# Kernel optimization log

Hardware: AMD Instinct MI355X
Metric: run time of the kernel (lower is better)

Reference implementation:

```python
import jax, jax.numpy as jnp
import numpy as np

N_NODES = 25000
N_EDGES = 50000
NUM_ATOMS = 26
HID = 64
EMB = 64
N_GRAPHS = 64
NUM_NN_ITER = 3


def setup_inputs() -> dict:
    key = jax.random.key(0)
    ks = jax.random.split(key, 16)

    def nrm(k, shape, s=0.1):
        return jax.random.normal(k, shape, dtype=jnp.float32) * s

    x = jax.random.uniform(ks[0], (N_NODES, NUM_ATOMS), dtype=jnp.float32)
    edge_index = jax.random.randint(ks[1], (2, N_EDGES), 0, N_NODES)
    edge_attr = jax.random.uniform(ks[2], (N_EDGES, 4), dtype=jnp.float32)
    batch = jnp.sort(jax.random.randint(ks[3], (N_NODES,), 0, N_GRAPHS))

    params = dict(
        W_in=nrm(ks[4], (NUM_ATOMS, HID)), b_in=jnp.zeros((HID,), jnp.float32),
        We1=nrm(ks[5], (4, 128)), be1=jnp.zeros((128,), jnp.float32),
        We2=nrm(ks[6], (128, HID * HID), 0.02), be2=jnp.zeros((HID * HID,), jnp.float32),
        W_root=nrm(ks[7], (HID, HID)), b_conv=jnp.zeros((HID,), jnp.float32),
        W_ih=nrm(ks[8], (3 * HID, HID)), b_ih=jnp.zeros((3 * HID,), jnp.float32),
        W_hh=nrm(ks[9], (3 * HID, HID)), b_hh=jnp.zeros((3 * HID,), jnp.float32),
        Wo1=nrm(ks[10], (HID, HID)), bo1=jnp.zeros((HID,), jnp.float32),
        Wo2=nrm(ks[11], (HID, EMB)), bo2=jnp.zeros((EMB,), jnp.float32),
        Wp=nrm(ks[12], (EMB + NUM_ATOMS, 1)), bp=jnp.zeros((1,), jnp.float32),
    )
    return {"x": x, "edge_index": edge_index, "edge_attr": edge_attr, "batch": batch, **params}


def reference(x, edge_index, edge_attr, batch,
              W_in, b_in, We1, be1, We2, be2, W_root, b_conv,
              W_ih, b_ih, W_hh, b_hh, Wo1, bo1, Wo2, bo2, Wp, bp):
    src, dst = edge_index[0], edge_index[1]
    # edge MLP -> per-edge (HID, HID) weight blocks; edge_attr is fixed so compute once
    Wedge = (jax.nn.relu(edge_attr @ We1 + be1) @ We2 + be2).reshape(-1, HID, HID)  # (E, h, h)

    out = jax.nn.relu(x @ W_in + b_in)  # (N, h)
    h = out
    for _ in range(NUM_NN_ITER):
        # NNConv (aggr='add'): root transform + gather->bmm->scatter_add
        msg = jnp.einsum('ei,eio->eo', out[src], Wedge)           # (E, h)
        agg = jax.ops.segment_sum(msg, dst, num_segments=N_NODES)  # (N, h)
        m = jax.nn.relu(out @ W_root + agg + b_conv)
        # single-step GRU cell (torch GRU equations)
        gi = m @ W_ih.T + b_ih
        gh = h @ W_hh.T + b_hh
        i_r, i_z, i_n = jnp.split(gi, 3, axis=-1)
        h_r, h_z, h_n = jnp.split(gh, 3, axis=-1)
        r = jax.nn.sigmoid(i_r + h_r)
        z = jax.nn.sigmoid(i_z + h_z)
        n = jnp.tanh(i_n + r * h_n)
        h = (1.0 - z) * n + z * h
        out = h

    o = jax.nn.relu(out @ Wo1 + bo1) @ Wo2 + bo2            # (N, EMB)
    feat = jnp.concatenate([o, x], axis=1)                  # (N, EMB + NUM_ATOMS)
    # F.normalize: row-wise L2 with eps clamp
    feat = feat / jnp.maximum(jnp.linalg.norm(feat, axis=1, keepdims=True), 1e-12)
    # scatter_mean readout over graphs
    cnt = jax.ops.segment_sum(jnp.ones((N_NODES,), jnp.float32), batch, num_segments=N_GRAPHS)
    readout = jax.ops.segment_sum(feat, batch, num_segments=N_GRAPHS) / jnp.maximum(cnt, 1.0)[:, None]
    ratio = jax.nn.sigmoid(readout @ Wp + bp)               # (G, 1)
    return feat, ratio
```

## Files before the change

kernel.cpp:

```cpp
#include <hip/hip_runtime.h>
#include <math.h>

#define NN 25000
#define NE 50000
#define NEP2 50176
#define NATOM 26
#define NUM_ITER 3
#define NCH 33
#define NPB 32
#define EB2 512
#define KSP 17

typedef __attribute__((ext_vector_type(8))) short bf16x8;
typedef __attribute__((ext_vector_type(8))) unsigned short ushort8_t;
typedef __attribute__((ext_vector_type(4))) float f32x4;
union FragU { bf16x8 v; ushort4 q[2]; };

static __device__ __forceinline__ ushort f2bf(float f) {
  unsigned u = __float_as_uint(f);
  unsigned r = (u + 0x7FFFu + ((u >> 16) & 1u)) >> 16;
  return (ushort)r;
}
static __device__ __forceinline__ unsigned cvt_pk_bf16(float a, float b) {
  unsigned r;
  asm("v_cvt_pk_bf16_f32 %0, %1, %2" : "=v"(r) : "v"(a), "v"(b));
  return r;
}
static __device__ __forceinline__ float bflo(unsigned u) { return __uint_as_float(u << 16); }
static __device__ __forceinline__ float bfhi(unsigned u) { return __uint_as_float(u & 0xFFFF0000u); }

__global__ __launch_bounds__(256) void edge_mlp_pack_kernel(
    const float* __restrict__ ea, const float* __restrict__ We1,
    const float* __restrict__ be1, ushort* __restrict__ Upkt) {
  int t = threadIdx.x;
  int el = t & 63, seg = t >> 6;
  int e = blockIdx.x * 64 + el;
  bool valid = (e < NE);
  float a0 = 0.f, a1 = 0.f, a2 = 0.f, a3 = 0.f;
  if (valid) { a0 = ea[e * 4]; a1 = ea[e * 4 + 1]; a2 = ea[e * 4 + 2]; a3 = ea[e * 4 + 3]; }
  #pragma unroll
  for (int q = 0; q < 8; ++q) {
    int g = seg * 8 + q;
    ushort out[4];
    #pragma unroll
    for (int kk = 0; kk < 4; ++kk) {
      int k = g * 4 + kk;
      float v = be1[k];
      v = fmaf(a0, We1[k], v);
      v = fmaf(a1, We1[128 + k], v);
      v = fmaf(a2, We1[256 + k], v);
      v = fmaf(a3, We1[384 + k], v);
      out[kk] = valid ? f2bf(fmaxf(v, 0.f)) : (ushort)0;
    }
    *(ushort4*)&Upkt[((size_t)g * NEP2 + e) * 4] = *(ushort4*)out;
  }
  if (seg == 0) {
    ushort out[4] = {(ushort)(valid ? 0x3F80 : 0), 0, 0, 0};
    *(ushort4*)&Upkt[((size_t)32 * NEP2 + e) * 4] = *(ushort4*)out;
  }
}

__global__ __launch_bounds__(256) void bpk_pack_kernel(
    const float* __restrict__ We2, const float* __restrict__ be2,
    ushort* __restrict__ Bpk) {
  int idx = blockIdx.x * 256 + threadIdx.x;
  int lane = idx & 63;
  int nt = (idx >> 6) & 3;
  int ks = (idx >> 8) & 7;
  int c = idx >> 11;
  int l15 = lane & 15, lg = lane >> 4;
  int o = nt * 16 + l15;
  ushort v[8];
  #pragma unroll
  for (int j = 0; j < 8; ++j) {
    int kl = (j < 4) ? (4 * lg + j) : (12 + 4 * lg + j);
    int f = c * 256 + ks * 32 + kl;
    int k = f >> 6, i = f & 63;
    float wv = 0.f;
    if (k < 128) wv = We2[(size_t)k * 4096 + i * 64 + o];
    else if (k == 128) wv = be2[i * 64 + o];
    v[j] = f2bf(wv);
  }
  *(ushort8_t*)(Bpk + (size_t)idx * 8) = *(ushort8_t*)v;
}

__global__ __launch_bounds__(256) void nw_pack_kernel(
    const float* __restrict__ W_root, const float* __restrict__ W_ih,
    const float* __restrict__ W_hh, ushort* __restrict__ Wr_pk,
    ushort* __restrict__ Bih_pk, ushort* __restrict__ Bhh_pk) {
  int idx = blockIdx.x * 256 + threadIdx.x;
  if (idx >= 3584) return;
  int lane, nt, ks, kind;
  ushort* dstp;
  if (idx < 512)      { kind = 0; int f = idx;        lane = f & 63; nt = (f >> 6) % 4;  ks = (f >> 6) / 4;  dstp = Wr_pk  + (size_t)f * 8; }
  else if (idx < 2048){ kind = 1; int f = idx - 512;  lane = f & 63; nt = (f >> 6) % 12; ks = (f >> 6) / 12; dstp = Bih_pk + (size_t)f * 8; }
  else                { kind = 2; int f = idx - 2048; lane = f & 63; nt = (f >> 6) % 12; ks = (f >> 6) / 12; dstp = Bhh_pk + (size_t)f * 8; }
  int l15 = lane & 15, lg = lane >> 4;
  int col = nt * 16 + l15;
  ushort v[8];
  #pragma unroll
  for (int j = 0; j < 8; ++j) {
    int kl = (j < 4) ? (4 * lg + j) : (12 + 4 * lg + j);
    int i = ks * 32 + kl;
    float wv;
    if (kind == 0)      wv = W_root[i * 64 + col];
    else if (kind == 1) wv = W_ih[col * 64 + i];
    else                wv = W_hh[col * 64 + i];
    v[j] = f2bf(wv);
  }
  *(ushort8_t*)dstp = *(ushort8_t*)v;
}

__global__ __launch_bounds__(512, 2) void edge_rgemm2_kernel(
    const ushort* __restrict__ Upkt, const ushort* __restrict__ Bpk,
    const float* __restrict__ hv, const int* __restrict__ src,
    const int* __restrict__ dst, float* __restrict__ agg) {
  __shared__ ushort sB[2][16384];
  __shared__ ushort sU[2][2048];
  __shared__ ushort sS[512][72];
  int tid = threadIdx.x;
  int lane = tid & 63, w = tid >> 6;
  int l15 = lane & 15, lg = lane >> 4;
  int e0 = blockIdx.x * EB2;
  int c0 = blockIdx.y * KSP;
  int c1 = (c0 + KSP < NCH) ? (c0 + KSP) : NCH;

  #pragma unroll
  for (int r = 0; r < 16; ++r) {
    int idx = r * 512 + tid;
    int el = idx >> 4, part = idx & 15;
    int e = e0 + el;
    float4 v = make_float4(0.f, 0.f, 0.f, 0.f);
    if (e < NE) v = ((const float4*)hv)[(size_t)src[e] * 16 + part];
    unsigned lo = cvt_pk_bf16(v.x, v.y);
    unsigned hi = cvt_pk_bf16(v.z, v.w);
    *(uint2*)&sS[el][part * 4] = make_uint2(lo, hi);
  }

  ushort8_t rB[4]; uint2 rU;
  {
    const ushort* bs = Bpk + (size_t)c0 * 16384;
    #pragma unroll
    for (int r = 0; r < 4; ++r)
      rB[r] = *(const ushort8_t*)(bs + ((size_t)r * 512 + tid) * 8);
    rU = *(const uint2*)(Upkt + ((size_t)c0 * NEP2 + e0) * 4 + tid * 4);
  }
  #pragma unroll
  for (int r = 0; r < 4; ++r)
    *(ushort8_t*)&sB[0][((size_t)r * 512 + tid) * 8] = rB[r];
  *(uint2*)&sU[0][tid * 4] = rU;
  __syncthreads();

  float4 sreg[4][2][2];
  #pragma unroll
  for (int mt = 0; mt < 4; ++mt)
    #pragma unroll
    for (int p = 0; p < 2; ++p)
      #pragma unroll
      for (int g = 0; g < 2; ++g) {
        uint2 d = *(const uint2*)&sS[w * 64 + mt * 16 + l15][p * 32 + g * 16 + 4 * lg];
        sreg[mt][p][g] = make_float4(bflo(d.x), bfhi(d.x), bflo(d.y), bfhi(d.y));
      }

  f32x4 acc[4][4];
  #pragma unroll
  for (int mt = 0; mt < 4; ++mt)
    #pragma unroll
    for (int nt = 0; nt < 4; ++nt) acc[mt][nt] = (f32x4){0.f, 0.f, 0.f, 0.f};

  for (int c = c0; c < c1; ++c) {
    int cur = (c - c0) & 1;
    bool more = (c + 1 < c1);
    if (more) {
      const ushort* bs = Bpk + (size_t)(c + 1) * 16384;
      #pragma unroll
      for (int r = 0; r < 4; ++r)
        rB[r] = *(const ushort8_t*)(bs + ((size_t)r * 512 + tid) * 8);
      rU = *(const uint2*)(Upkt + ((size_t)(c + 1) * NEP2 + e0) * 4 + tid * 4);
    }
    float uu[4][4];
    #pragma unroll
    for (int mt = 0; mt < 4; ++mt) {
      uint2 d = *(const uint2*)&sU[cur][(w * 64 + mt * 16 + l15) * 4];
      uu[mt][0] = bflo(d.x); uu[mt][1] = bfhi(d.x);
      uu[mt][2] = bflo(d.y); uu[mt][3] = bfhi(d.y);
    }
    #pragma unroll
    for (int ks = 0; ks < 8; ++ks) {
      int p = ks & 1, ku = ks >> 1;
      bf16x8 bfr[4];
      #pragma unroll
      for (int nt = 0; nt < 4; ++nt)
        bfr[nt] = *(const bf16x8*)&sB[cur][(((size_t)ks * 4 + nt) * 64 + lane) * 8];
      #pragma unroll
      for (int mt = 0; mt < 4; ++mt) {
        float u = uu[mt][ku];
        float4 s0 = sreg[mt][p][0], s1 = sreg[mt][p][1];
        union { bf16x8 v; unsigned u32[4]; } af;
        af.u32[0] = cvt_pk_bf16(s0.x * u, s0.y * u);
        af.u32[1] = cvt_pk_bf16(s0.z * u, s0.w * u);
        af.u32[2] = cvt_pk_bf16(s1.x * u, s1.y * u);
        af.u32[3] = cvt_pk_bf16(s1.z * u, s1.w * u);
        #pragma unroll
        for (int nt = 0; nt < 4; ++nt)
          acc[mt][nt] = __builtin_amdgcn_mfma_f32_16x16x32_bf16(af.v, bfr[nt], acc[mt][nt], 0, 0, 0);
      }
    }
    if (more) {
      int nb = cur ^ 1;
      #pragma unroll
      for (int r = 0; r < 4; ++r)
        *(ushort8_t*)&sB[nb][((size_t)r * 512 + tid) * 8] = rB[r];
      *(uint2*)&sU[nb][tid * 4] = rU;
    }
    __syncthreads();
  }

  #pragma unroll
  for (int mt = 0; mt < 4; ++mt) {
    #pragma unroll
    for (int rr = 0; rr < 4; ++rr) {
      int e = e0 + w * 64 + mt * 16 + lg * 4 + rr;
      if (e < NE) {
        int d = dst[e];
        #pragma unroll
        for (int nt = 0; nt < 4; ++nt)
          atomicAdd(&agg[(size_t)d * 64 + nt * 16 + l15], acc[mt][nt][rr]);
      }
    }
  }
}

__global__ __launch_bounds__(256) void node_in_kernel(
    const float* __restrict__ x, const float* __restrict__ W_in,
    const float* __restrict__ b_in, float* __restrict__ h) {
  int idx = blockIdx.x * 256 + threadIdx.x;
  if (idx >= NN * 64) return;
  int n = idx >> 6, c = idx & 63;
  float acc = b_in[c];
  #pragma unroll
  for (int j = 0; j < NATOM; ++j) acc = fmaf(x[n * NATOM + j], W_in[j * 64 + c], acc);
  h[idx] = fmaxf(acc, 0.f);
}

__global__ __launch_bounds__(256, 1) void node_update2_kernel(
    float* __restrict__ hv, const float* __restrict__ agg,
    const ushort* __restrict__ Wr_pk, const ushort* __restrict__ Bih_pk,
    const ushort* __restrict__ Bhh_pk, const float* __restrict__ b_conv,
    const float* __restrict__ b_ih, const float* __restrict__ b_hh) {
  __shared__ ushort h_lds[128][72];
  __shared__ ushort m_lds[128][72];
  int tid = threadIdx.x;
  int lane = tid & 63, w = tid >> 6;
  int l15 = lane & 15, lg = lane >> 4;
  int n0 = blockIdx.x * 128;

  #pragma unroll
  for (int r = 0; r < 8; ++r) {
    int idx = r * 256 + tid;
    int row = idx >> 4, part = idx & 15;
    int n = n0 + row;
    float4 v = make_float4(0.f, 0.f, 0.f, 0.f);
    if (n < NN) v = ((const float4*)hv)[(size_t)n * 16 + part];
    *(uint2*)&h_lds[row][part * 4] =
        make_uint2(cvt_pk_bf16(v.x, v.y), cvt_pk_bf16(v.z, v.w));
  }
  __syncthreads();

  bf16x8 ah[2][2];
  #pragma unroll
  for (int mt = 0; mt < 2; ++mt)
    #pragma unroll
    for (int ks = 0; ks < 2; ++ks) {
      int row = w * 32 + mt * 16 + l15;
      FragU f;
      f.q[0] = *(const ushort4*)&h_lds[row][ks * 32 + 4 * lg];
      f.q[1] = *(const ushort4*)&h_lds[row][ks * 32 + 16 + 4 * lg];
      ah[mt][ks] = f.v;
    }

  f32x4 accm[2][4];
  #pragma unroll
  for (int mt = 0; mt < 2; ++mt)
    #pragma unroll
    for (int nt = 0; nt < 4; ++nt) accm[mt][nt] = (f32x4){0.f, 0.f, 0.f, 0.f};
  #pragma unroll
  for (int ks = 0; ks < 2; ++ks)
    #pragma unroll
    for (int nt = 0; nt < 4; ++nt) {
      bf16x8 b = *(const bf16x8*)(Wr_pk + ((size_t)((ks * 4 + nt) * 64 + lane)) * 8);
      #pragma unroll
      for (int mt = 0; mt < 2; ++mt)
        accm[mt][nt] = __builtin_amdgcn_mfma_f32_16x16x32_bf16(ah[mt][ks], b, accm[mt][nt], 0, 0, 0);
    }
  #pragma unroll
  for (int mt = 0; mt < 2; ++mt)
    #pragma unroll
    for (int nt = 0; nt < 4; ++nt) {
      int col = nt * 16 + l15;
      float bc = b_conv[col];
      #pragma unroll
      for (int rr = 0; rr < 4; ++rr) {
        int row = w * 32 + mt * 16 + lg * 4 + rr;
        int n = n0 + row;
        float val = 0.f;
        if (n < NN) val = fmaxf(accm[mt][nt][rr] + agg[(size_t)n * 64 + col] + bc, 0.f);
        m_lds[row][col] = f2bf(val);
      }
    }
  __syncthreads();

  bf16x8 am[2][2];
  #pragma unroll
  for (int mt = 0; mt < 2; ++mt)
    #pragma unroll
    for (int ks = 0; ks < 2; ++ks) {
      int row = w * 32 + mt * 16 + l15;
      FragU f;
      f.q[0] = *(const ushort4*)&m_lds[row][ks * 32 + 4 * lg];
      f.q[1] = *(const ushort4*)&m_lds[row][ks * 32 + 16 + 4 * lg];
      am[mt][ks] = f.v;
    }

  f32x4 acc_s[2][8], acc_in[2][4], acc_hn[2][4];
  #pragma unroll
  for (int mt = 0; mt < 2; ++mt) {
    #pragma unroll
    for (int nt = 0; nt < 8; ++nt) acc_s[mt][nt] = (f32x4){0.f, 0.f, 0.f, 0.f};
    #pragma unroll
    for (int nt = 0; nt < 4; ++nt) {
      acc_in[mt][nt] = (f32x4){0.f, 0.f, 0.f, 0.f};
      acc_hn[mt][nt] = (f32x4){0.f, 0.f, 0.f, 0.f};
    }
  }
  #pragma unroll
  for (int ks = 0; ks < 2; ++ks) {
    #pragma unroll
    for (int nt = 0; nt < 8; ++nt) {
      bf16x8 bi = *(const bf16x8*)(Bih_pk + ((size_t)((ks * 12 + nt) * 64 + lane)) * 8);
      bf16x8 bh = *(const bf16x8*)(Bhh_pk + ((size_t)((ks * 12 + nt) * 64 + lane)) * 8);
      #pragma unroll
      for (int mt = 0; mt < 2; ++mt) {
        acc_s[mt][nt] = __builtin_amdgcn_mfma_f32_16x16x32_bf16(am[mt][ks], bi, acc_s[mt][nt], 0, 0, 0);
        acc_s[mt][nt] = __builtin_amdgcn_mfma_f32_16x16x32_bf16(ah[mt][ks], bh, acc_s[mt][nt], 0, 0, 0);
      }
    }
    #pragma unroll
    for (int nt = 8; nt < 12; ++nt) {
      bf16x8 bi = *(const bf16x8*)(Bih_pk + ((size_t)((ks * 12 + nt) * 64 + lane)) * 8);
      bf16x8 bh = *(const bf16x8*)(Bhh_pk + ((size_t)((ks * 12 + nt) * 64 + lane)) * 8);
      #pragma unroll
      for (int mt = 0; mt < 2; ++mt) {
        acc_in[mt][nt - 8] = __builtin_amdgcn_mfma_f32_16x16x32_bf16(am[mt][ks], bi, acc_in[mt][nt - 8], 0, 0, 0);
        acc_hn[mt][nt - 8] = __builtin_amdgcn_mfma_f32_16x16x32_bf16(ah[mt][ks], bh, acc_hn[mt][nt - 8], 0, 0, 0);
      }
    }
  }

  #pragma unroll
  for (int mt = 0; mt < 2; ++mt)
    #pragma unroll
    for (int nt = 0; nt < 4; ++nt) {
      int col = nt * 16 + l15;
      float b_sr = b_ih[col] + b_hh[col];
      float b_sz = b_ih[64 + col] + b_hh[64 + col];
      float b_in_ = b_ih[128 + col];
      float b_hn = b_hh[128 + col];
      #pragma unroll
      for (int rr = 0; rr < 4; ++rr) {
        int row = w * 32 + mt * 16 + lg * 4 + rr;
        int n = n0 + row;
        if (n >= NN) continue;
        float Sr = acc_s[mt][nt][rr] + b_sr;
        float Sz = acc_s[mt][nt + 4][rr] + b_sz;
        float vin = acc_in[mt][nt][rr] + b_in_;
        float vhn = acc_hn[mt][nt][rr] + b_hn;
        float r = 1.f / (1.f + __expf(-Sr));
        float z = 1.f / (1.f + __expf(-Sz));
        float nn = tanhf(fmaf(r, vhn, vin));
        float hp = hv[(size_t)n * 64 + col];
        hv[(size_t)n * 64 + col] = (1.f - z) * nn + z * hp;
      }
    }
}

__global__ __launch_bounds__(256) void head2_kernel(
    const float* __restrict__ hv, const float* __restrict__ x,
    const float* __restrict__ Wo1, const float* __restrict__ bo1,
    const float* __restrict__ Wo2, const float* __restrict__ bo2,
    float* __restrict__ feat) {
  __shared__ float wo1[64 * 64];
  __shared__ float wo2[64 * 64];
  __shared__ float s_row[NPB * 64];
  __shared__ float s_o1[NPB * 64];
  int tid = threadIdx.x;
  int n0 = blockIdx.x * NPB;

  for (int idx = tid; idx < 64 * 16; idx += 256) {
    ((float4*)wo1)[idx] = ((const float4*)Wo1)[idx];
    ((float4*)wo2)[idx] = ((const float4*)Wo2)[idx];
  }
  for (int idx = tid; idx < NPB * 64; idx += 256) {
    int n = n0 + (idx >> 6);
    s_row[idx] = (n < NN) ? hv[(size_t)n * 64 + (idx & 63)] : 0.f;
  }
  __syncthreads();

  int c = tid & 63, g = tid >> 6;
  #pragma unroll
  for (int q = 0; q < 8; ++q) {
    int nl = g + 4 * q;
    float a = bo1[c];
    for (int i = 0; i < 64; ++i) a = fmaf(s_row[nl * 64 + i], wo1[i * 64 + c], a);
    s_o1[nl * 64 + c] = fmaxf(a, 0.f);
  }
  __syncthreads();
  #pragma unroll
  for (int q = 0; q < 8; ++q) {
    int nl = g + 4 * q;
    int n = n0 + nl;
    float b = bo2[c];
    for (int i = 0; i < 64; ++i) b = fmaf(s_o1[nl * 64 + i], wo2[i * 64 + c], b);
    float xv = (c < NATOM && n < NN) ? x[(size_t)n * NATOM + c] : 0.f;
    float sq = b * b + xv * xv;
    #pragma unroll
    for (int off = 1; off < 64; off <<= 1) sq += __shfl_xor(sq, off);
    if (n >= NN) continue;
    float inv = 1.f / fmaxf(sqrtf(sq), 1e-12f);
    feat[(size_t)n * 90 + c] = b * inv;
    if (c < NATOM) feat[(size_t)n * 90 + 64 + c] = xv * inv;
  }
}

static __device__ __forceinline__ int lbound(const int* __restrict__ b, int v) {
  int lo = 0, hi = NN;
  while (lo < hi) { int m = (lo + hi) >> 1; if (b[m] < v) lo = m + 1; else hi = m; }
  return lo;
}

__global__ __launch_bounds__(128) void readout_kernel(
    const float* __restrict__ feat, const int* __restrict__ batch,
    float* __restrict__ readout, float* __restrict__ cnt) {
  __shared__ int bounds[2];
  int g = blockIdx.x;
  int t = threadIdx.x;
  if (t == 0) bounds[0] = lbound(batch, g);
  if (t == 1) bounds[1] = lbound(batch, g + 1);
  __syncthreads();
  int lo = bounds[0], hi = bounds[1];
  if (t < 90) {
    float a0 = 0.f, a1 = 0.f, a2 = 0.f, a3 = 0.f;
    int n = lo;
    for (; n + 3 < hi; n += 4) {
      a0 += feat[(size_t)n * 90 + t];
      a1 += feat[(size_t)(n + 1) * 90 + t];
      a2 += feat[(size_t)(n + 2) * 90 + t];
      a3 += feat[(size_t)(n + 3) * 90 + t];
    }
    for (; n < hi; ++n) a0 += feat[(size_t)n * 90 + t];
    readout[g * 90 + t] = (a0 + a1) + (a2 + a3);
  }
  if (t == 0) cnt[g] = (float)(hi - lo);
}

__global__ __launch_bounds__(64) void ratio_kernel(
    const float* __restrict__ readout, const float* __restrict__ cnt,
    const float* __restrict__ Wp, const float* __restrict__ bp,
    float* __restrict__ ratio) {
  int g = threadIdx.x;
  float c = fmaxf(cnt[g], 1.f);
  float a = bp[0];
  for (int j = 0; j < 90; ++j) a = fmaf(readout[g * 90 + j] / c, Wp[j], a);
  ratio[g] = 1.f / (1.f + __expf(-a));
}


extern "C" void kernel_launch(void* const* d_in, const int* in_sizes, int n_in,
                              void* d_out, int out_size, void* d_ws, size_t ws_size,
                              hipStream_t stream) {
  const float* x      = (const float*)d_in[0];
  const int*   ei     = (const int*)  d_in[1];
  const float* ea     = (const float*)d_in[2];
  const int*   batch  = (const int*)  d_in[3];
  const float* W_in   = (const float*)d_in[4];
  const float* b_in   = (const float*)d_in[5];
  const float* We1    = (const float*)d_in[6];
  const float* be1    = (const float*)d_in[7];
  const float* We2    = (const float*)d_in[8];
  const float* be2    = (const float*)d_in[9];
  const float* W_root = (const float*)d_in[10];
  const float* b_conv = (const float*)d_in[11];
  const float* W_ih   = (const float*)d_in[12];
  const float* b_ih   = (const float*)d_in[13];
  const float* W_hh   = (const float*)d_in[14];
  const float* b_hh   = (const float*)d_in[15];
  const float* Wo1    = (const float*)d_in[16];
  const float* bo1    = (const float*)d_in[17];
  const float* Wo2    = (const float*)d_in[18];
  const float* bo2    = (const float*)d_in[19];
  const float* Wp     = (const float*)d_in[20];
  const float* bp     = (const float*)d_in[21];

  const int* srcp = ei;
  const int* dstp = ei + NE;
  float* feat  = (float*)d_out;
  float* ratio = feat + (size_t)NN * 90;

  char* wsb = (char*)d_ws;
  ushort* Upkt   = (ushort*)(wsb + 0);
  ushort* Bpk    = (ushort*)(wsb + 13246464);
  float*  h      = (float*) (wsb + 14327808);
  float*  agg    = (float*) (wsb + 20727808);
  float*  readout= (float*) (wsb + 27127808);
  float*  cnt    = (float*) (wsb + 27150848);
  ushort* Wr_pk  = (ushort*)(wsb + 27151104);
  ushort* Bih_pk = (ushort*)(wsb + 27159296);
  ushort* Bhh_pk = (ushort*)(wsb + 27183872);

  edge_mlp_pack_kernel<<<NEP2 / 64, 256, 0, stream>>>(ea, We1, be1, Upkt);
  bpk_pack_kernel<<<(NCH * 8 * 4 * 64) / 256, 256, 0, stream>>>(We2, be2, Bpk);
  nw_pack_kernel<<<14, 256, 0, stream>>>(W_root, W_ih, W_hh, Wr_pk, Bih_pk, Bhh_pk);
  node_in_kernel<<<(NN * 64 + 255) / 256, 256, 0, stream>>>(x, W_in, b_in, h);

  for (int it = 0; it < NUM_ITER; ++it) {
    hipMemsetAsync(agg, 0, (size_t)NN * 64 * sizeof(float), stream);
    edge_rgemm2_kernel<<<dim3(NEP2 / EB2, 2), 512, 0, stream>>>(
        Upkt, Bpk, h, srcp, dstp, agg);
    node_update2_kernel<<<(NN + 127) / 128, 256, 0, stream>>>(
        h, agg, Wr_pk, Bih_pk, Bhh_pk, b_conv, b_ih, b_hh);
  }

  head2_kernel<<<(NN + NPB - 1) / NPB, 256, 0, stream>>>(
      h, x, Wo1, bo1, Wo2, bo2, feat);
  readout_kernel<<<64, 128, 0, stream>>>(feat, batch, readout, cnt);
  ratio_kernel<<<1, 64, 0, stream>>>(readout, cnt, Wp, bp, ratio);
}
```

Measured before the change: 441.6 us.

## Restructure edge GEMM: factor U scaling out of MFMA, split output columns, async LDS loads

The edge-conditioned GEMM kernel is reorganised. Source features are converted to bf16 fragments once, kept in registers, and reused as MFMA A operands. The per-edge U coefficient is applied as an fp32 FMA on the MFMA result, which removes the per-k rescale and bf16 conversion of A. Output columns are split across a new grid z dimension so each block handles 32 columns, halving LDS and accumulator use and allowing 4 blocks per CU. B tiles are double-buffered with global_load_lds, and U is read straight from global memory. The cost is twice as many MFMAs per useful output (two chained MFMAs plus an FMA per tile), a doubled source-row gather across the column halves, and extra fp32 FMAs.

```diff
diff --git a/kernel.cpp b/kernel.cpp
--- a/kernel.cpp
+++ b/kernel.cpp
@@ -15,6 +15,10 @@
 typedef __attribute__((ext_vector_type(8))) unsigned short ushort8_t;
 typedef __attribute__((ext_vector_type(4))) float f32x4;
 union FragU { bf16x8 v; ushort4 q[2]; };
+
+#define GLDS16(gp, lp) __builtin_amdgcn_global_load_lds( \
+    (const __attribute__((address_space(1))) void*)(gp), \
+    (__attribute__((address_space(3))) void*)(lp), 16, 0, 0)
 
 static __device__ __forceinline__ ushort f2bf(float f) {
   unsigned u = __float_as_uint(f);
@@ -111,107 +115,94 @@
   *(ushort8_t*)dstp = *(ushort8_t*)v;
 }
 
-__global__ __launch_bounds__(512, 2) void edge_rgemm2_kernel(
+__global__ __launch_bounds__(512, 4) void edge_rgemm5_kernel(
     const ushort* __restrict__ Upkt, const ushort* __restrict__ Bpk,
     const float* __restrict__ hv, const int* __restrict__ src,
     const int* __restrict__ dst, float* __restrict__ agg) {
-  __shared__ ushort sB[2][16384];
-  __shared__ ushort sU[2][2048];
-  __shared__ ushort sS[512][72];
+  __shared__ ushort sB[2][8192];
   int tid = threadIdx.x;
   int lane = tid & 63, w = tid >> 6;
   int l15 = lane & 15, lg = lane >> 4;
   int e0 = blockIdx.x * EB2;
   int c0 = blockIdx.y * KSP;
   int c1 = (c0 + KSP < NCH) ? (c0 + KSP) : NCH;
-
-  #pragma unroll
-  for (int r = 0; r < 16; ++r) {
-    int idx = r * 512 + tid;
-    int el = idx >> 4, part = idx & 15;
-    int e = e0 + el;
-    float4 v = make_float4(0.f, 0.f, 0.f, 0.f);
-    if (e < NE) v = ((const float4*)hv)[(size_t)src[e] * 16 + part];
-    unsigned lo = cvt_pk_bf16(v.x, v.y);
-    unsigned hi = cvt_pk_bf16(v.z, v.w);
-    *(uint2*)&sS[el][part * 4] = make_uint2(lo, hi);
-  }
-
-  ushort8_t rB[4]; uint2 rU;
+  int nh = blockIdx.z;
+
   {
-    const ushort* bs = Bpk + (size_t)c0 * 16384;
-    #pragma unroll
-    for (int r = 0; r < 4; ++r)
-      rB[r] = *(const ushort8_t*)(bs + ((size_t)r * 512 + tid) * 8);
-    rU = *(const uint2*)(Upkt + ((size_t)c0 * NEP2 + e0) * 4 + tid * 4);
-  }
-  #pragma unroll
-  for (int r = 0; r < 4; ++r)
-    *(ushort8_t*)&sB[0][((size_t)r * 512 + tid) * 8] = rB[r];
-  *(uint2*)&sU[0][tid * 4] = rU;
+    const ushort* bs = Bpk + ((((size_t)c0 * 8 + w) * 4 + nh * 2) * 64) * 8;
+    GLDS16(bs + (size_t)lane * 8, &sB[0][(size_t)(w * 128) * 8]);
+    GLDS16(bs + (size_t)(64 + lane) * 8, &sB[0][(size_t)(w * 128 + 64) * 8]);
+  }
+
+  bf16x8 sfr[4][2];
+  #pragma unroll
+  for (int mt = 0; mt < 4; ++mt) {
+    int e = e0 + w * 64 + mt * 16 + l15;
+    int es = (e < NE) ? e : (NE - 1);
+    const float* hp = hv + (size_t)src[es] * 64;
+    #pragma unroll
+    for (int p = 0; p < 2; ++p) {
+      float4 a = *(const float4*)(hp + p * 32 + 4 * lg);
+      float4 b = *(const float4*)(hp + p * 32 + 16 + 4 * lg);
+      union { bf16x8 v; unsigned u[4]; } f;
+      f.u[0] = cvt_pk_bf16(a.x, a.y);
+      f.u[1] = cvt_pk_bf16(a.z, a.w);
+      f.u[2] = cvt_pk_bf16(b.x, b.y);
+      f.u[3] = cvt_pk_bf16(b.z, b.w);
+      sfr[mt][p] = f.v;
+    }
+  }
+  f32x4 kZ = (f32x4){0.f, 0.f, 0.f, 0.f};
+
+  f32x4 acc[4][2];
+  #pragma unroll
+  for (int mt = 0; mt < 4; ++mt)
+    #pragma unroll
+    for (int nt = 0; nt < 2; ++nt) acc[mt][nt] = (f32x4){0.f, 0.f, 0.f, 0.f};
   __syncthreads();
-
-  float4 sreg[4][2][2];
-  #pragma unroll
-  for (int mt = 0; mt < 4; ++mt)
-    #pragma unroll
-    for (int p = 0; p < 2; ++p)
-      #pragma unroll
-      for (int g = 0; g < 2; ++g) {
-        uint2 d = *(const uint2*)&sS[w * 64 + mt * 16 + l15][p * 32 + g * 16 + 4 * lg];
-        sreg[mt][p][g] = make_float4(bflo(d.x), bfhi(d.x), bflo(d.y), bfhi(d.y));
-      }
-
-  f32x4 acc[4][4];
-  #pragma unroll
-  for (int mt = 0; mt < 4; ++mt)
-    #pragma unroll
-    for (int nt = 0; nt < 4; ++nt) acc[mt][nt] = (f32x4){0.f, 0.f, 0.f, 0.f};
 
   for (int c = c0; c < c1; ++c) {
     int cur = (c - c0) & 1;
-    bool more = (c + 1 < c1);
-    if (more) {
-      const ushort* bs = Bpk + (size_t)(c + 1) * 16384;
-      #pragma unroll
-      for (int r = 0; r < 4; ++r)
-        rB[r] = *(const ushort8_t*)(bs + ((size_t)r * 512 + tid) * 8);
-      rU = *(const uint2*)(Upkt + ((size_t)(c + 1) * NEP2 + e0) * 4 + tid * 4);
-    }
-    float uu[4][4];
-    #pragma unroll
-    for (int mt = 0; mt < 4; ++mt) {
-      uint2 d = *(const uint2*)&sU[cur][(w * 64 + mt * 16 + l15) * 4];
-      uu[mt][0] = bflo(d.x); uu[mt][1] = bfhi(d.x);
-      uu[mt][2] = bflo(d.y); uu[mt][3] = bfhi(d.y);
-    }
-    #pragma unroll
-    for (int ks = 0; ks < 8; ++ks) {
-      int p = ks & 1, ku = ks >> 1;
-      bf16x8 bfr[4];
-      #pragma unroll
-      for (int nt = 0; nt < 4; ++nt)
-        bfr[nt] = *(const bf16x8*)&sB[cur][(((size_t)ks * 4 + nt) * 64 + lane) * 8];
+    if (c + 1 < c1) {
+      const ushort* bs = Bpk + ((((size_t)(c + 1) * 8 + w) * 4 + nh * 2) * 64) * 8;
+      GLDS16(bs + (size_t)lane * 8, &sB[cur ^ 1][(size_t)(w * 128) * 8]);
+      GLDS16(bs + (size_t)(64 + lane) * 8, &sB[cur ^ 1][(size_t)(w * 128 + 64) * 8]);
+    }
+    #pragma unroll
+    for (int kup = 0; kup < 2; ++kup) {
+      unsigned uw[4][4];
       #pragma unroll
       for (int mt = 0; mt < 4; ++mt) {
-        float u = uu[mt][ku];
-        float4 s0 = sreg[mt][p][0], s1 = sreg[mt][p][1];
-        union { bf16x8 v; unsigned u32[4]; } af;
-        af.u32[0] = cvt_pk_bf16(s0.x * u, s0.y * u);
-        af.u32[1] = cvt_pk_bf16(s0.z * u, s0.w * u);
-        af.u32[2] = cvt_pk_bf16(s1.x * u, s1.y * u);
-        af.u32[3] = cvt_pk_bf16(s1.z * u, s1.w * u);
+        const ushort* up = Upkt + ((size_t)c * NEP2 + e0 + w * 64 + mt * 16 + lg * 4) * 4 + kup * 2;
         #pragma unroll
-        for (int nt = 0; nt < 4; ++nt)
-          acc[mt][nt] = __builtin_amdgcn_mfma_f32_16x16x32_bf16(af.v, bfr[nt], acc[mt][nt], 0, 0, 0);
-      }
-    }
-    if (more) {
-      int nb = cur ^ 1;
-      #pragma unroll
-      for (int r = 0; r < 4; ++r)
-        *(ushort8_t*)&sB[nb][((size_t)r * 512 + tid) * 8] = rB[r];
-      *(uint2*)&sU[nb][tid * 4] = rU;
+        for (int rr = 0; rr < 4; ++rr)
+          uw[mt][rr] = *(const unsigned*)(up + rr * 4);
+      }
+      #pragma unroll
+      for (int kh = 0; kh < 2; ++kh) {
+        int ku = kup * 2 + kh;
+        bf16x8 b0[2], b1[2];
+        #pragma unroll
+        for (int nt = 0; nt < 2; ++nt) {
+          b0[nt] = *(const bf16x8*)&sB[cur][(((size_t)(2 * ku) * 128) + nt * 64 + lane) * 8];
+          b1[nt] = *(const bf16x8*)&sB[cur][(((size_t)(2 * ku + 1) * 128) + nt * 64 + lane) * 8];
+        }
+        #pragma unroll
+        for (int mt = 0; mt < 4; ++mt) {
+          float uf[4];
+          #pragma unroll
+          for (int rr = 0; rr < 4; ++rr)
+            uf[rr] = kh ? bfhi(uw[mt][rr]) : bflo(uw[mt][rr]);
+          #pragma unroll
+          for (int nt = 0; nt < 2; ++nt) {
+            f32x4 t = __builtin_amdgcn_mfma_f32_16x16x32_bf16(sfr[mt][0], b0[nt], kZ, 0, 0, 0);
+            t = __builtin_amdgcn_mfma_f32_16x16x32_bf16(sfr[mt][1], b1[nt], t, 0, 0, 0);
+            #pragma unroll
+            for (int rr = 0; rr < 4; ++rr)
+              acc[mt][nt][rr] = fmaf(uf[rr], t[rr], acc[mt][nt][rr]);
+          }
+        }
+      }
     }
     __syncthreads();
   }
@@ -224,8 +215,8 @@
       if (e < NE) {
         int d = dst[e];
         #pragma unroll
-        for (int nt = 0; nt < 4; ++nt)
-          atomicAdd(&agg[(size_t)d * 64 + nt * 16 + l15], acc[mt][nt][rr]);
+        for (int nt = 0; nt < 2; ++nt)
+          atomicAdd(&agg[(size_t)d * 64 + nh * 32 + nt * 16 + l15], acc[mt][nt][rr]);
       }
     }
   }
@@ -524,7 +515,7 @@
 
   for (int it = 0; it < NUM_ITER; ++it) {
     hipMemsetAsync(agg, 0, (size_t)NN * 64 * sizeof(float), stream);
-    edge_rgemm2_kernel<<<dim3(NEP2 / EB2, 2), 512, 0, stream>>>(
+    edge_rgemm5_kernel<<<dim3(NEP2 / EB2, 2, 2), 512, 0, stream>>>(
         Upkt, Bpk, h, srcp, dstp, agg);
     node_update2_kernel<<<(NN + 127) / 128, 256, 0, stream>>>(
         h, agg, Wr_pk, Bih_pk, Bhh_pk, b_conv, b_ih, b_hh);
```

Result: slower. 986.6 us (+123.4%).
